# Performance work log

Measured on AMD Instinct MI355X. Metric: run time of the kernel, lower is better.

The kernel has to match this reference:

```python
import jax, jax.numpy as jnp
import numpy as np

EMB = 1024
HEADS = 16
HEAD_DIM = EMB // HEADS
B, S = 4, 2048


def setup_inputs() -> dict:
    key = jax.random.key(0)
    ks = jax.random.split(key, 7)
    sc = 1.0 / np.sqrt(EMB)
    return {
        "query": jax.random.normal(ks[0], (B, S, EMB), jnp.float32),
        "key": jax.random.normal(ks[1], (B, S, EMB), jnp.float32),
        "value": jax.random.normal(ks[2], (B, S, EMB), jnp.float32),
        "Wq": jax.random.normal(ks[3], (EMB, EMB), jnp.float32) * sc,
        "Wk": jax.random.normal(ks[4], (EMB, EMB), jnp.float32) * sc,
        "Wv": jax.random.normal(ks[5], (EMB, EMB), jnp.float32) * sc,
        "Wo": jax.random.normal(ks[6], (EMB, EMB), jnp.float32) * sc,
    }


def reference(query, key, value, Wq, Wk, Wv, Wo):
    # nn.Linear applies x @ W^T; W stored as [out, in]
    def split_heads(x):  # [B,S,E] -> [B,H,S,D]
        return x.reshape(B, -1, HEADS, HEAD_DIM).transpose(0, 2, 1, 3)

    q = split_heads(query @ Wq.T)
    k = split_heads(key @ Wk.T)
    v = split_heads(value @ Wv.T)
    scores = jnp.einsum('bhse,bhte->bhst', q, k) / np.sqrt(HEAD_DIM).astype(np.float32)
    attn = jax.nn.softmax(scores, axis=-1)
    ctx = jnp.einsum('bhst,bhtd->bshd', attn, v)  # [B,S,H,D]
    out = ctx.reshape(B, -1, EMB) @ Wo.T
    return out
```

## Files before the change

### kernel.cpp

```cpp
#include <hip/hip_runtime.h>
#include <hip/hip_bf16.h>

#define EMB   1024
#define HEADS 16
#define HDIM  64
#define BB    4
#define SS    2048
#define MROWS (BB*SS)

typedef __bf16 bf16_t;
typedef __bf16 bf16x4_t __attribute__((ext_vector_type(4)));
typedef __bf16 bf16x8   __attribute__((ext_vector_type(8)));
typedef float  f32x4    __attribute__((ext_vector_type(4)));

__device__ __forceinline__ void glds16(const void* g, void* l) {
  __builtin_amdgcn_global_load_lds(
      (const __attribute__((address_space(1))) void*)g,
      (__attribute__((address_space(3))) void*)l, 16, 0, 0);
}

__launch_bounds__(256)
__global__ void cast_multi(const float* s0, const float* s1, const float* s2,
                           const float* s3, const float* s4, const float* s5,
                           const float* s6,
                           bf16_t* d0, bf16_t* d1, bf16_t* d2, bf16_t* d3,
                           bf16_t* d4, bf16_t* d5, bf16_t* d6, int nact) {
  const int z = blockIdx.z;
  if (z >= nact && blockIdx.x >= 512) return;
  const float* ss[7] = {s0, s1, s2, s3, s4, s5, s6};
  bf16_t*      dd[7] = {d0, d1, d2, d3, d4, d5, d6};
  const float* s = ss[z];
  bf16_t*      d = dd[z];
  const int i = (blockIdx.x*256 + threadIdx.x) * 8;
  const f32x4 a = *(const f32x4*)&s[i];
  const f32x4 b = *(const f32x4*)&s[i+4];
  bf16x8 r;
  r[0]=(bf16_t)a[0]; r[1]=(bf16_t)a[1]; r[2]=(bf16_t)a[2]; r[3]=(bf16_t)a[3];
  r[4]=(bf16_t)b[0]; r[5]=(bf16_t)b[1]; r[6]=(bf16_t)b[2]; r[7]=(bf16_t)b[3];
  *(bf16x8*)&d[i] = r;
}

__launch_bounds__(256)
__global__ void cast_f32_bf16(const float* __restrict__ src, bf16_t* __restrict__ dst) {
  const int i = (blockIdx.x*256 + threadIdx.x) * 8;
  const f32x4 a = *(const f32x4*)&src[i];
  const f32x4 b = *(const f32x4*)&src[i+4];
  bf16x8 r;
  r[0]=(bf16_t)a[0]; r[1]=(bf16_t)a[1]; r[2]=(bf16_t)a[2]; r[3]=(bf16_t)a[3];
  r[4]=(bf16_t)b[0]; r[5]=(bf16_t)b[1]; r[6]=(bf16_t)b[2]; r[7]=(bf16_t)b[3];
  *(bf16x8*)&dst[i] = r;
}

__device__ __forceinline__ void gemm_core(const bf16_t* __restrict__ A,
                                          const bf16_t* __restrict__ W,
                                          bf16_t* As, bf16_t* Bs,
                                          f32x4 acc[4][4],
                                          int bm0, int bn0,
                                          int wave, int lane) {
  const int quad = lane >> 4, l16 = lane & 15;
  const int wm = wave >> 1, wn = wave & 1;
  for (int k0 = 0; k0 < EMB; k0 += 32) {
#pragma unroll
    for (int j = 0; j < 2; ++j) {
      const int i   = wave*2 + j;
      const int row = i*16 + (lane >> 2);
      const int col = (lane & 3) * 8;
      glds16(A + (size_t)(bm0 + row)*EMB + k0 + col, &As[i*512]);
      glds16(W + (size_t)(bn0 + row)*EMB + k0 + col, &Bs[i*512]);
    }
    __syncthreads();

    bf16x8 a[4], b[4];
#pragma unroll
    for (int t = 0; t < 4; ++t) {
      a[t] = *(const bf16x8*)&As[(wm*64 + t*16 + l16)*32 + quad*8];
      b[t] = *(const bf16x8*)&Bs[(wn*64 + t*16 + l16)*32 + quad*8];
    }
#pragma unroll
    for (int mt = 0; mt < 4; ++mt)
#pragma unroll
      for (int nt = 0; nt < 4; ++nt)
        acc[mt][nt] = __builtin_amdgcn_mfma_f32_16x16x32_bf16(a[mt], b[nt], acc[mt][nt], 0, 0, 0);
    __syncthreads();
  }
}

__launch_bounds__(256)
__global__ void gemm_qkv(const bf16_t* A0, const bf16_t* A1, const bf16_t* A2,
                         const bf16_t* W0, const bf16_t* W1, const bf16_t* W2,
                         bf16_t* C0, bf16_t* C1, bf16_t* C2,
                         float sscale, int zbase) {
  __shared__ __align__(16) bf16_t As[128*32];
  __shared__ __align__(16) bf16_t Bs[128*32];
  const int tid  = threadIdx.x;
  const int wave = tid >> 6, lane = tid & 63;
  const int quad = lane >> 4, l16 = lane & 15;
  const int wm = wave >> 1, wn = wave & 1;

  const int fid = blockIdx.x + 8*(blockIdx.y + 64*blockIdx.z);
  const int xcd = fid & 7, s = fid >> 3;
  const int bn0 = (s & 7) * 128;
  const int p   = xcd + 8*(s >> 3);
  const int z   = (p >> 6) + zbase;
  const int bm0 = (p & 63) * 128;

  const bf16_t* A = (z == 0) ? A0 : (z == 1) ? A1 : A2;
  const bf16_t* W = (z == 0) ? W0 : (z == 1) ? W1 : W2;
  bf16_t*       C = (z == 0) ? C0 : (z == 1) ? C1 : C2;
  const float oscale = (z == 0) ? sscale : 1.0f;

  f32x4 acc[4][4] = {};
  gemm_core(A, W, As, Bs, acc, bm0, bn0, wave, lane);

  if (z == 2) {
    const int bb = bm0 >> 11;
    const int T  = ((bm0 & 2047) >> 6) + wm;
    const int h  = (bn0 >> 6) + wn;
    bf16_t* base = C + ((size_t)(bb*HEADS + h)*32 + T)*4096;
#pragma unroll
    for (int ks = 0; ks < 2; ++ks)
#pragma unroll
      for (int nt = 0; nt < 4; ++nt) {
        bf16x8 v;
#pragma unroll
        for (int r = 0; r < 4; ++r) {
          v[r]     = (bf16_t)acc[2*ks][nt][r];
          v[4 + r] = (bf16_t)acc[2*ks + 1][nt][r];
        }
        *(bf16x8*)&base[((nt*2 + ks)*64 + quad*16 + l16)*8] = v;
      }
  } else {
#pragma unroll
    for (int mt = 0; mt < 4; ++mt) {
      const int row = bm0 + wm*64 + mt*16 + quad*4;
#pragma unroll
      for (int nt = 0; nt < 4; ++nt) {
        const int col = bn0 + wn*64 + nt*16 + l16;
#pragma unroll
        for (int r = 0; r < 4; ++r)
          C[(size_t)(row + r)*EMB + col] = (bf16_t)(acc[mt][nt][r] * oscale);
      }
    }
  }
}

__launch_bounds__(256)
__global__ void gemm_out(const bf16_t* __restrict__ A, const bf16_t* __restrict__ W,
                         float* __restrict__ C) {
  __shared__ __align__(16) bf16_t As[128*32];
  __shared__ __align__(16) bf16_t Bs[128*32];
  const int tid  = threadIdx.x;
  const int wave = tid >> 6, lane = tid & 63;
  const int quad = lane >> 4, l16 = lane & 15;
  const int wm = wave >> 1, wn = wave & 1;

  const int fid = blockIdx.x + 8*blockIdx.y;
  const int xcd = fid & 7, s = fid >> 3;
  const int bn0 = (s & 7) * 128;
  const int bm0 = (xcd*8 + (s >> 3)) * 128;

  f32x4 acc[4][4] = {};
  gemm_core(A, W, As, Bs, acc, bm0, bn0, wave, lane);

#pragma unroll
  for (int mt = 0; mt < 4; ++mt) {
    const int row = bm0 + wm*64 + mt*16 + quad*4;
#pragma unroll
    for (int nt = 0; nt < 4; ++nt) {
      const int col = bn0 + wn*64 + nt*16 + l16;
#pragma unroll
      for (int r = 0; r < 4; ++r)
        C[(size_t)(row + r)*EMB + col] = acc[mt][nt][r];
    }
  }
}

__launch_bounds__(256)
__global__ void attn(const bf16_t* Qp, const bf16_t* __restrict__ Kp,
                     const bf16_t* __restrict__ Vt, bf16_t* Cx) {
  __shared__ __align__(16) bf16_t Ks[2*64*32];
  __shared__ __align__(16) bf16_t Vs[4096];

  const int tid  = threadIdx.x;
  const int wave = tid >> 6, lane = tid & 63;
  const int quad = lane >> 4, l16 = lane & 15;

  const int fid  = blockIdx.x + 16*(blockIdx.y + 16*blockIdx.z);
  const int xcd  = fid & 7, s = fid >> 3;
  const int q0   = (s & 15) * 128;
  const int pair = xcd*8 + (s >> 4);
  const int h    = pair & 15;
  const int b    = pair >> 4;

  bf16x8 qf[2][2];
#pragma unroll
  for (int mb = 0; mb < 2; ++mb) {
    const size_t qr = (size_t)(b*SS + q0 + wave*32 + mb*16 + l16)*EMB + h*HDIM;
#pragma unroll
    for (int ks = 0; ks < 2; ++ks)
      qf[mb][ks] = *(const bf16x8*)&Qp[qr + ks*32 + quad*8];
  }

  const bf16_t* Kb = Kp + (size_t)b*SS*EMB + h*HDIM;
  const bf16_t* Vb = Vt + ((size_t)(b*HEADS + h)*32)*4096;

  f32x4 o[2][4] = {};
  float lsum[2] = {0.f, 0.f};

  for (int t0 = 0; t0 < SS; t0 += 64) {
#pragma unroll
    for (int c = 0; c < 2; ++c) {
      const int i   = wave + c*4;
      const int r   = (i & 3)*16 + (lane >> 2);
      const int col = (lane & 3)*8;
      glds16(Kb + (size_t)(t0 + r)*EMB + c*32 + col, &Ks[i*512]);
      glds16(Vb + (size_t)(t0 >> 6)*4096 + i*512 + lane*8, &Vs[i*512]);
    }
    __syncthreads();

    f32x4 st[2][4] = {};
#pragma unroll
    for (int cb = 0; cb < 4; ++cb) {
      const bf16x8 kf0 = *(const bf16x8*)&Ks[(cb*16 + l16)*32 + quad*8];
      const bf16x8 kf1 = *(const bf16x8*)&Ks[2048 + (cb*16 + l16)*32 + quad*8];
#pragma unroll
      for (int mb = 0; mb < 2; ++mb) {
        st[mb][cb] = __builtin_amdgcn_mfma_f32_16x16x32_bf16(kf0, qf[mb][0], st[mb][cb], 0, 0, 0);
        st[mb][cb] = __builtin_amdgcn_mfma_f32_16x16x32_bf16(kf1, qf[mb][1], st[mb][cb], 0, 0, 0);
      }
    }

    bf16x8 pb[2][2];
#pragma unroll
    for (int mb = 0; mb < 2; ++mb) {
      float ls = 0.f;
#pragma unroll
      for (int kb = 0; kb < 4; ++kb)
#pragma unroll
        for (int r = 0; r < 4; ++r) {
          const float p = __builtin_amdgcn_exp2f(st[mb][kb][r]);
          st[mb][kb][r] = p;
          ls += p;
        }
      lsum[mb] += ls;
#pragma unroll
      for (int ks = 0; ks < 2; ++ks)
#pragma unroll
        for (int r = 0; r < 4; ++r) {
          pb[mb][ks][r]     = (bf16_t)st[mb][2*ks][r];
          pb[mb][ks][4 + r] = (bf16_t)st[mb][2*ks + 1][r];
        }
    }

#pragma unroll
    for (int ks = 0; ks < 2; ++ks)
#pragma unroll
      for (int dt = 0; dt < 4; ++dt) {
        const bf16x8 vf = *(const bf16x8*)&Vs[((dt*2 + ks)*64 + quad*16 + l16)*8];
#pragma unroll
        for (int mb = 0; mb < 2; ++mb)
          o[mb][dt] = __builtin_amdgcn_mfma_f32_16x16x32_bf16(vf, pb[mb][ks], o[mb][dt], 0, 0, 0);
      }
    __syncthreads();
  }

#pragma unroll
  for (int mb = 0; mb < 2; ++mb) {
    float l = lsum[mb];
    l += __shfl_xor(l, 16, 64);
    l += __shfl_xor(l, 32, 64);
    const float inv = 1.0f / l;
    const size_t row = (size_t)(b*SS + q0 + wave*32 + mb*16 + l16)*EMB + h*HDIM;
#pragma unroll
    for (int dt = 0; dt < 4; ++dt) {
      bf16x4_t v;
#pragma unroll
      for (int r = 0; r < 4; ++r) v[r] = (bf16_t)(o[mb][dt][r] * inv);
      *(bf16x4_t*)&Cx[row + dt*16 + quad*4] = v;
    }
  }
}

extern "C" void kernel_launch(void* const* d_in, const int* in_sizes, int n_in,
                              void* d_out, int out_size, void* d_ws, size_t ws_size,
                              hipStream_t stream) {
  (void)in_sizes; (void)n_in; (void)out_size;
  const float* query = (const float*)d_in[0];
  const float* key   = (const float*)d_in[1];
  const float* value = (const float*)d_in[2];
  const float* WqF   = (const float*)d_in[3];
  const float* WkF   = (const float*)d_in[4];
  const float* WvF   = (const float*)d_in[5];
  const float* WoF   = (const float*)d_in[6];

  const size_t AN = (size_t)MROWS*EMB;
  const size_t WN = (size_t)EMB*EMB;
  float* out = (float*)d_out;
  bf16_t* S5 = (bf16_t*)d_out;
  bf16_t* S6 = S5 + AN;

  const float sscale = 0.125f * 1.44269504f;

  const dim3 gqkv(EMB/128, MROWS/128, 3);
  const dim3 gqk (EMB/128, MROWS/128, 2);
  const dim3 gv  (EMB/128, MROWS/128, 1);
  const dim3 gg  (EMB/128, MROWS/128);
  const dim3 gattn(SS/128, HEADS, BB);

  if (ws_size >= (size_t)(4*AN + 4*WN) * sizeof(bf16_t)) {
    bf16_t* qb  = (bf16_t*)d_ws;
    bf16_t* kb  = qb + AN;
    bf16_t* vb  = kb + AN;
    bf16_t* S2  = vb + AN;
    bf16_t* Wqb = S2 + AN;
    bf16_t* Wkb = Wqb + WN;
    bf16_t* Wvb = Wkb + WN;
    bf16_t* Wob = Wvb + WN;

    cast_multi<<<dim3(AN/2048, 1, 7), 256, 0, stream>>>(
        query, key, value, WqF, WkF, WvF, WoF,
        qb, kb, vb, Wqb, Wkb, Wvb, Wob, 3);
    gemm_qkv<<<gqkv, 256, 0, stream>>>(qb, kb, vb, Wqb, Wkb, Wvb,
                                       S2, S6, S5, sscale, 0);
    attn<<<gattn, 256, 0, stream>>>(S2, S6, S5, S2);
    gemm_out<<<gg, 256, 0, stream>>>(S2, Wob, out);
  } else {
    bf16_t* S1  = (bf16_t*)d_ws;
    bf16_t* S2  = S1 + AN;
    bf16_t* Wqb = S2 + AN;
    bf16_t* Wkb = Wqb + WN;
    bf16_t* Wvb = Wkb + WN;
    bf16_t* Wob = Wvb + WN;

    cast_multi<<<dim3(AN/2048, 1, 6), 256, 0, stream>>>(
        query, key, WqF, WkF, WvF, WoF, WoF,
        S1, S5, Wqb, Wkb, Wvb, Wob, Wob, 2);
    gemm_qkv<<<gqk, 256, 0, stream>>>(S1, S5, S1, Wqb, Wkb, Wvb,
                                      S2, S6, S5, sscale, 0);
    cast_f32_bf16<<<dim3(AN/2048), 256, 0, stream>>>(value, S1);
    gemm_qkv<<<gv, 256, 0, stream>>>(S1, S1, S1, Wvb, Wvb, Wvb,
                                     S5, S5, S5, 1.0f, 2);
    attn<<<gattn, 256, 0, stream>>>(S2, S6, S5, S2);
    gemm_out<<<gg, 256, 0, stream>>>(S2, Wob, out);
  }
}
```

Baseline: 330.2 us.

## Double-buffer K/V tiles in attention loop with a single barrier per iteration

Splits the K and V shared-memory tiles into two buffers and issues the global-to-LDS loads for the next 64-key tile before computing on the current one. This lets load latency overlap with the MFMA work and removes the trailing barrier in each iteration. The K LDS layout is remapped so each lane reads a contiguous 16-byte chunk, and the row-sum of exponentials is kept in a vector accumulator with the horizontal reduction moved to the end. The cost is double the LDS use per block, which may lower occupancy.

```diff
diff --git a/kernel.cpp b/kernel.cpp
--- a/kernel.cpp
+++ b/kernel.cpp
@@ -178,8 +178,8 @@
 __launch_bounds__(256)
 __global__ void attn(const bf16_t* Qp, const bf16_t* __restrict__ Kp,
                      const bf16_t* __restrict__ Vt, bf16_t* Cx) {
-  __shared__ __align__(16) bf16_t Ks[2*64*32];
-  __shared__ __align__(16) bf16_t Vs[4096];
+  __shared__ __align__(16) bf16_t Ks[2][4096];
+  __shared__ __align__(16) bf16_t Vs[2][4096];
 
   const int tid  = threadIdx.x;
   const int wave = tid >> 6, lane = tid & 63;
@@ -205,24 +205,29 @@
   const bf16_t* Vb = Vt + ((size_t)(b*HEADS + h)*32)*4096;
 
   f32x4 o[2][4] = {};
-  float lsum[2] = {0.f, 0.f};
-
-  for (int t0 = 0; t0 < SS; t0 += 64) {
+  f32x4 lsv[2] = {};
+
+  auto stage = [&](int t0, int bf) {
 #pragma unroll
     for (int c = 0; c < 2; ++c) {
-      const int i   = wave + c*4;
-      const int r   = (i & 3)*16 + (lane >> 2);
-      const int col = (lane & 3)*8;
-      glds16(Kb + (size_t)(t0 + r)*EMB + c*32 + col, &Ks[i*512]);
-      glds16(Vb + (size_t)(t0 >> 6)*4096 + i*512 + lane*8, &Vs[i*512]);
-    }
+      const int i = wave + c*4;
+      glds16(Kb + (size_t)(t0 + (i&3)*16 + l16)*EMB + (i>>2)*32 + quad*8,
+             &Ks[bf][i*512]);
+      glds16(Vb + (size_t)(t0 >> 6)*4096 + i*512 + lane*8, &Vs[bf][i*512]);
+    }
+  };
+
+  stage(0, 0);
+
+  for (int t0 = 0, buf = 0; t0 < SS; t0 += 64, buf ^= 1) {
     __syncthreads();
+    if (t0 + 64 < SS) stage(t0 + 64, buf ^ 1);
 
     f32x4 st[2][4] = {};
 #pragma unroll
     for (int cb = 0; cb < 4; ++cb) {
-      const bf16x8 kf0 = *(const bf16x8*)&Ks[(cb*16 + l16)*32 + quad*8];
-      const bf16x8 kf1 = *(const bf16x8*)&Ks[2048 + (cb*16 + l16)*32 + quad*8];
+      const bf16x8 kf0 = *(const bf16x8*)&Ks[buf][cb*512 + lane*8];
+      const bf16x8 kf1 = *(const bf16x8*)&Ks[buf][2048 + cb*512 + lane*8];
 #pragma unroll
       for (int mb = 0; mb < 2; ++mb) {
         st[mb][cb] = __builtin_amdgcn_mfma_f32_16x16x32_bf16(kf0, qf[mb][0], st[mb][cb], 0, 0, 0);
@@ -233,16 +238,13 @@
     bf16x8 pb[2][2];
 #pragma unroll
     for (int mb = 0; mb < 2; ++mb) {
-      float ls = 0.f;
-#pragma unroll
-      for (int kb = 0; kb < 4; ++kb)
-#pragma unroll
-        for (int r = 0; r < 4; ++r) {
-          const float p = __builtin_amdgcn_exp2f(st[mb][kb][r]);
-          st[mb][kb][r] = p;
-          ls += p;
-        }
-      lsum[mb] += ls;
+#pragma unroll
+      for (int kb = 0; kb < 4; ++kb) {
+#pragma unroll
+        for (int r = 0; r < 4; ++r)
+          st[mb][kb][r] = __builtin_amdgcn_exp2f(st[mb][kb][r]);
+        lsv[mb] += st[mb][kb];
+      }
 #pragma unroll
       for (int ks = 0; ks < 2; ++ks)
 #pragma unroll
@@ -256,17 +258,16 @@
     for (int ks = 0; ks < 2; ++ks)
 #pragma unroll
       for (int dt = 0; dt < 4; ++dt) {
-        const bf16x8 vf = *(const bf16x8*)&Vs[((dt*2 + ks)*64 + quad*16 + l16)*8];
+        const bf16x8 vf = *(const bf16x8*)&Vs[buf][((dt*2 + ks)*64 + lane)*8];
 #pragma unroll
         for (int mb = 0; mb < 2; ++mb)
           o[mb][dt] = __builtin_amdgcn_mfma_f32_16x16x32_bf16(vf, pb[mb][ks], o[mb][dt], 0, 0, 0);
       }
-    __syncthreads();
   }
 
 #pragma unroll
   for (int mb = 0; mb < 2; ++mb) {
-    float l = lsum[mb];
+    float l = lsv[mb][0] + lsv[mb][1] + lsv[mb][2] + lsv[mb][3];
     l += __shfl_xor(l, 16, 64);
     l += __shfl_xor(l, 32, 64);
     const float inv = 1.0f / l;
```

Result: faster. 321.6 us (-2.6%).
